# Kernel tuning notes

Hardware: AMD Instinct MI355X
Metric: run time of the kernel (lower is better)

The kernel has to match this reference:

```python
import jax, jax.numpy as jnp
import numpy as np

B, C, H, W = 16, 192, 56, 56
WS = 7; L = WS * WS; NH = 8; HD = C // NH
SHIFTS = (0, 3, 0, 3)  # shift = 0 if i%2==0 else window_size//2


def _ln(x, g, b):
    m = jnp.mean(x, -1, keepdims=True)
    v = jnp.var(x, -1, keepdims=True)
    return (x - m) * jax.lax.rsqrt(v + 1e-5) * g + b


def _win_part(x):
    # (b, H, W, c) -> (b*nW, L, c)
    b, c = x.shape[0], x.shape[-1]
    x = x.reshape(b, H // WS, WS, W // WS, WS, c).transpose(0, 1, 3, 2, 4, 5)
    return x.reshape(-1, L, c)


def _win_rev(xw, b):
    # (b*nW, L, c) -> (b, H, W, c)
    c = xw.shape[-1]
    x = xw.reshape(b, H // WS, W // WS, WS, WS, c).transpose(0, 1, 3, 2, 4, 5)
    return x.reshape(b, H, W, c)


def _rel_index():
    co = np.stack(np.meshgrid(np.arange(WS), np.arange(WS), indexing='ij')).reshape(2, -1)
    r = (co[:, :, None] - co[:, None, :]).transpose(1, 2, 0).astype(np.int64)
    r[..., 0] += WS - 1; r[..., 1] += WS - 1; r[..., 0] *= 2 * WS - 1
    return r.sum(-1)  # (L, L)

REL_IDX = _rel_index()


def _mask(shift):
    if shift == 0:
        return None
    img = np.zeros((1, H, W, 1), np.float32)
    cnt = 0.0
    sl = (slice(0, H - WS), slice(H - WS, H - shift), slice(H - shift, None))
    for hs in sl:
        for ws_ in sl:
            img[:, hs, ws_, :] = cnt
            cnt += 1.0
    mw = np.asarray(_win_part(jnp.asarray(img))).reshape(-1, L)
    am = mw[:, None, :] - mw[:, :, None]
    return jnp.asarray(np.where(am != 0, -100.0, 0.0).astype(np.float32))  # (nW, L, L)

MASKS = [_mask(s) for s in SHIFTS]


def _block(x, n1g, n1b, qw, qb, pw, pb, tab, n2g, n2b, f1w, f1b, f2w, f2b, shift, mask):
    b = x.shape[0]
    sc = x
    x = _ln(x, n1g, n1b)
    if shift:
        x = jnp.roll(x, (-shift, -shift), (1, 2))
    xw = _win_part(x)  # (b*nW, L, C)
    qkv = (xw @ qw.T + qb).reshape(-1, L, 3, NH, HD).transpose(2, 0, 3, 1, 4)
    q, k, v = qkv[0], qkv[1], qkv[2]  # (nB, NH, L, HD)
    attn = jnp.einsum('bhid,bhjd->bhij', q * (HD ** -0.5), k)
    attn = attn + tab[REL_IDX].transpose(2, 0, 1)  # relative position bias (NH, L, L)
    if mask is not None:
        nW = mask.shape[0]
        attn = (attn.reshape(b, nW, NH, L, L) + mask[None, :, None]).reshape(-1, NH, L, L)
    attn = jax.nn.softmax(attn, -1)
    out = jnp.einsum('bhij,bhjd->bhid', attn, v).transpose(0, 2, 1, 3).reshape(-1, L, C)
    out = out @ pw.T + pb
    x = _win_rev(out, b)
    if shift:
        x = jnp.roll(x, (shift, shift), (1, 2))
    x = sc + x
    y = _ln(x, n2g, n2b)
    y = jax.nn.gelu(y @ f1w.T + f1b, approximate=False) @ f2w.T + f2b
    return x + y


def _conv_bn_relu(x, w, b, g, bt, m, v):
    x = jax.lax.conv_general_dilated(x, w, (1, 1), ((1, 1), (1, 1)),
                                     dimension_numbers=('NCHW', 'OIHW', 'NCHW'))
    x = x + b[None, :, None, None]
    x = (x - m[None, :, None, None]) * jax.lax.rsqrt(v + 1e-5)[None, :, None, None]
    x = x * g[None, :, None, None] + bt[None, :, None, None]
    return jax.nn.relu(x)


def setup_inputs() -> dict:
    key = jax.random.key(0)
    ks = iter(jax.random.split(key, 48))
    rn = lambda shape, s=0.02: jax.random.normal(next(ks), shape, jnp.float32) * s
    OD = 96
    return dict(
        x=jax.random.normal(next(ks), (B, C, H, W), jnp.float32),
        pos_embed=rn((1, H * W, C)),
        proj_w=rn((C, C)), proj_b=jnp.zeros((C,)),
        pe_g=jnp.ones((C,)), pe_b=jnp.zeros((C,)),
        n1_g=jnp.ones((4, C)), n1_b=jnp.zeros((4, C)),
        qkv_w=rn((4, 3 * C, C)), qkv_b=jnp.zeros((4, 3 * C)),
        attn_pw=rn((4, C, C)), attn_pb=jnp.zeros((4, C)),
        rel_tab=rn((4, (2 * WS - 1) ** 2, NH)),
        n2_g=jnp.ones((4, C)), n2_b=jnp.zeros((4, C)),
        fc1_w=rn((4, 4 * C, C)), fc1_b=jnp.zeros((4, 4 * C)),
        fc2_w=rn((4, C, 4 * C)), fc2_b=jnp.zeros((4, C)),
        c1_w=rn((C, C, 3, 3)), c1_b=jnp.zeros((C,)),
        bn1_g=jnp.ones((C,)), bn1_b=jnp.zeros((C,)), bn1_m=rn((C,), 0.1), bn1_v=jnp.ones((C,)),
        c2_w=rn((OD, C, 3, 3)), c2_b=jnp.zeros((OD,)),
        bn2_g=jnp.ones((OD,)), bn2_b=jnp.zeros((OD,)), bn2_m=rn((OD,), 0.1), bn2_v=jnp.ones((OD,)),
    )


def reference(x, pos_embed, proj_w, proj_b, pe_g, pe_b, n1_g, n1_b, qkv_w, qkv_b,
              attn_pw, attn_pb, rel_tab, n2_g, n2_b, fc1_w, fc1_b, fc2_w, fc2_b,
              c1_w, c1_b, bn1_g, bn1_b, bn1_m, bn1_v,
              c2_w, c2_b, bn2_g, bn2_b, bn2_m, bn2_v):
    # PatchEmbedding: 1x1 conv == per-pixel linear, then LN, + pos embed
    t = jnp.einsum('bchw,dc->bhwd', x, proj_w) + proj_b  # (B, H, W, D)
    t = _ln(t.reshape(B, H * W, C), pe_g, pe_b) + pos_embed
    o = t.reshape(B, H, W, C)
    for i in range(4):
        o = _block(o, n1_g[i], n1_b[i], qkv_w[i], qkv_b[i], attn_pw[i], attn_pb[i],
                   rel_tab[i], n2_g[i], n2_b[i], fc1_w[i], fc1_b[i], fc2_w[i], fc2_b[i],
                   SHIFTS[i], MASKS[i])
    ds2 = o.transpose(0, 3, 1, 2)  # (B, C, H, W)
    h1 = _conv_bn_relu(ds2, c1_w, c1_b, bn1_g, bn1_b, bn1_m, bn1_v)
    conv_out = _conv_bn_relu(h1, c2_w, c2_b, bn2_g, bn2_b, bn2_m, bn2_v)
    return (conv_out, ds2)
```

## Files before the change

kernel.cpp:

```cpp
#include <hip/hip_runtime.h>
#include <math.h>

typedef unsigned short u16;
typedef unsigned int u32;
typedef __attribute__((ext_vector_type(8))) short short8;
typedef __attribute__((ext_vector_type(4))) float f32x4;

#define IMG 56
#define HW_ 3136
#define NTOK 50176
#define C_DIM 192
#define CONV_OUT_SZ 4816896

__device__ inline float bf2f(u16 v) {
  u32 u = ((u32)v) << 16; float f; __builtin_memcpy(&f, &u, 4); return f;
}
__device__ inline u16 f2bf(float f) {
  u32 u; __builtin_memcpy(&u, &f, 4);
  u += 0x7FFF + ((u >> 16) & 1);
  return (u16)(u >> 16);
}
__device__ inline void glds16(const u16* g, u16* l) {
  __builtin_amdgcn_global_load_lds((const __attribute__((address_space(1))) u32*)g,
                                   (__attribute__((address_space(3))) u32*)l, 16, 0, 0);
}
__device__ inline u32 pk_bf16(float a, float b) {
  u32 r;
  asm("v_cvt_pk_bf16_f32 %0, %1, %2" : "=v"(r) : "v"(a), "v"(b));
  return r;
}

template<int AMODE, int EPI>
__global__ __launch_bounds__(256) void gmm(
    const u16* __restrict__ A, const u16* __restrict__ W,
    const float* __restrict__ bias, void* __restrict__ Cout,
    int M, int N, int K,
    const float* __restrict__ bg, const float* __restrict__ bb,
    const float* __restrict__ bm, const float* __restrict__ bv, int shiftp)
{
  __shared__ u16 As[128 * 64];
  __shared__ u16 Bs[64 * 64];
  const int tid = threadIdx.x;
  const int m0 = blockIdx.x * 128, n0 = blockIdx.y * 64;
  const int lane = tid & 63, wid = tid >> 6;
  const int wm = (wid >> 1) * 64, wn = (wid & 1) * 32;
  const int fr = lane & 15, fg = lane >> 4;
  f32x4 acc[4][2] = {};

  for (int kc = 0; kc < K; kc += 64) {
    #pragma unroll
    for (int it = 0; it < 2; ++it) {
      const int g = it * 256 + tid;
      const int row = g >> 3, cb = (g & 7) << 4;
      const int sc = cb ^ ((row & 7) << 4);
      glds16(W + (size_t)(n0 + row) * K + kc + (sc >> 1), Bs + g * 8);
    }
    if (AMODE == 0) {
      #pragma unroll
      for (int it = 0; it < 4; ++it) {
        const int g = it * 256 + tid;
        const int row = g >> 3, cb = (g & 7) << 4;
        const int sc = cb ^ ((row & 7) << 4);
        glds16(A + (size_t)(m0 + row) * K + kc + (sc >> 1), As + g * 8);
      }
    } else {
      #pragma unroll
      for (int it = 0; it < 4; ++it) {
        const int g = it * 256 + tid;
        const int row = g >> 3, cb = (g & 7) << 4;
        const int m = m0 + row;
        const int b = m / HW_, pp = m - b * HW_;
        const int y = pp / IMG, x = pp - (pp / IMG) * IMG;
        const int kg = kc + (cb >> 1);
        const int s = kg / C_DIM, ic = kg - s * C_DIM;
        const int yy = y + s / 3 - 1, xx = x + (s % 3) - 1;
        short8 v = {0, 0, 0, 0, 0, 0, 0, 0};
        if ((unsigned)yy < IMG && (unsigned)xx < IMG)
          v = *(const short8*)(A + ((size_t)(b * HW_ + yy * IMG + xx)) * C_DIM + ic);
        *(short8*)(As + row * 64 + ((cb ^ ((row & 7) << 4)) >> 1)) = v;
      }
    }
    __syncthreads();
    #pragma unroll
    for (int ks = 0; ks < 2; ++ks) {
      const int kb = ks * 64 + fg * 16;
      short8 af[4], bf[2];
      #pragma unroll
      for (int i = 0; i < 4; ++i) {
        const int row = wm + i * 16 + fr;
        af[i] = *(const short8*)(As + ((row * 128 + (kb ^ ((row & 7) << 4))) >> 1));
      }
      #pragma unroll
      for (int j = 0; j < 2; ++j) {
        const int row = wn + j * 16 + fr;
        bf[j] = *(const short8*)(Bs + ((row * 128 + (kb ^ ((row & 7) << 4))) >> 1));
      }
      #pragma unroll
      for (int i = 0; i < 4; ++i)
        #pragma unroll
        for (int j = 0; j < 2; ++j)
          acc[i][j] = __builtin_amdgcn_mfma_f32_16x16x32_bf16(af[i], bf[j], acc[i][j], 0, 0, 0);
    }
    __syncthreads();
  }

  const int c0 = n0 + wn + fr;
  const int c1i = (EPI == 4) ? min(c0 + 16, N - 1) : (c0 + 16);
  const float bias0 = bias[c0], bias1 = bias[c1i];
  float s0 = 0.f, h0 = 0.f, s1 = 0.f, h1 = 0.f;
  if (EPI == 3 || EPI == 4) {
    s0 = bg[c0] * rsqrtf(bv[c0] + 1e-5f); h0 = bb[c0] - bm[c0] * s0;
    s1 = bg[c1i] * rsqrtf(bv[c1i] + 1e-5f); h1 = bb[c1i] - bm[c1i] * s1;
  }
  #pragma unroll
  for (int i = 0; i < 4; ++i) {
    #pragma unroll
    for (int r = 0; r < 4; ++r) {
      const int m = m0 + wm + i * 16 + fg * 4 + r;
      size_t sbase = 0;
      if (EPI == 6) {
        const int wno = m / 49, within = m - wno * 49;
        const int b2 = wno >> 6, wb3 = wno & 63;
        const int wr = within / 7, wc = within - wr * 7;
        int y2 = (wb3 >> 3) * 7 + wr + shiftp; if (y2 >= IMG) y2 -= IMG;
        int x2 = (wb3 & 7) * 7 + wc + shiftp; if (x2 >= IMG) x2 -= IMG;
        sbase = ((size_t)(b2 * HW_ + y2 * IMG + x2)) * C_DIM;
      }
      #pragma unroll
      for (int j = 0; j < 2; ++j) {
        const int c = c0 + j * 16;
        float v = acc[i][j][r] + (j ? bias1 : bias0);
        if (EPI == 1) v = 0.5f * v * (1.f + erff(v * 0.70710678118f));
        if (EPI == 3 || EPI == 4) { v = v * (j ? s1 : s0) + (j ? h1 : h0); v = fmaxf(v, 0.f); }
        if (EPI == 0 || EPI == 1 || EPI == 3) {
          ((u16*)Cout)[(size_t)m * N + c] = f2bf(v);
        } else if (EPI == 5) {
          ((float*)Cout)[(size_t)m * N + c] = v;
        } else if (EPI == 2) {
          ((float*)Cout)[(size_t)m * N + c] += v;
        } else if (EPI == 6) {
          ((float*)Cout)[sbase + c] += v;
        } else {
          if (c < N) {
            const int b = m / HW_, pp = m - b * HW_;
            ((float*)Cout)[((size_t)b * N + c) * HW_ + pp] = v;
          }
        }
      }
    }
  }
}

__device__ inline void stv(float* p, float v) { *p = v; }
__device__ inline void stv(u16* p, float v) { *p = f2bf(v); }

template<typename OT>
__global__ __launch_bounds__(256) void ln_k(
    const float* __restrict__ in, OT* __restrict__ outp,
    const float* __restrict__ g, const float* __restrict__ bta,
    const float* __restrict__ pos, int winpart, int shift)
{
  const int t = blockIdx.x * 4 + (threadIdx.x >> 6);
  const int lane = threadIdx.x & 63;
  const float* xr = in + (size_t)t * C_DIM;
  const float v0 = xr[lane], v1 = xr[lane + 64], v2 = xr[lane + 128];
  float s = v0 + v1 + v2;
  float ss = v0 * v0 + v1 * v1 + v2 * v2;
  #pragma unroll
  for (int off = 32; off > 0; off >>= 1) {
    s += __shfl_xor(s, off);
    ss += __shfl_xor(ss, off);
  }
  const float mean = s * (1.f / 192.f);
  const float inv = rsqrtf(ss * (1.f / 192.f) - mean * mean + 1e-5f);
  const int b = t / HW_, pp = t - b * HW_;
  size_t obase;
  if (winpart) {
    const int y = pp / IMG, x = pp - (pp / IMG) * IMG;
    int yr = y - shift; if (yr < 0) yr += IMG;
    int xs = x - shift; if (xs < 0) xs += IMG;
    const int win = b * 64 + (yr / 7) * 8 + (xs / 7);
    const int within = (yr % 7) * 7 + (xs % 7);
    obase = ((size_t)win * 49 + within) * C_DIM;
  } else {
    obase = (size_t)t * C_DIM;
  }
  OT* o = outp + obase;
  float p0 = 0.f, p1 = 0.f, p2 = 0.f;
  if (pos) {
    const float* pr = pos + (size_t)pp * C_DIM;
    p0 = pr[lane]; p1 = pr[lane + 64]; p2 = pr[lane + 128];
  }
  stv(o + lane,       (v0 - mean) * inv * g[lane]       + bta[lane]       + p0);
  stv(o + lane + 64,  (v1 - mean) * inv * g[lane + 64]  + bta[lane + 64]  + p1);
  stv(o + lane + 128, (v2 - mean) * inv * g[lane + 128] + bta[lane + 128] + p2);
}

template<int SHIFT>
__global__ __launch_bounds__(256) void attn_m(
    const u16* __restrict__ qkv, u16* __restrict__ outp,
    const float* __restrict__ rel)
{
  __shared__ u16 VT[128 * 64];
  __shared__ float relS[4 * 176 + 16];
  const int tid = threadIdx.x;
  const int wid = tid >> 6, lane = tid & 63;
  const int fr = lane & 15, fg = lane >> 4;
  const int win = blockIdx.x >> 1;
  const int hb = blockIdx.x & 1;
  const int h = hb * 4 + wid;
  const u16* wbase = qkv + (size_t)win * 49 * 576;

  {
    u32* vz = (u32*)VT;
    #pragma unroll
    for (int it = 0; it < 16; ++it) vz[it * 256 + tid] = 0;
  }
  for (int id = tid; id < 169 * 4; id += 256) {
    const int hl = id & 3, ridx = id >> 2;
    relS[hl * 176 + ridx] = rel[ridx * 8 + hb * 4 + hl];
  }
  __syncthreads();
  for (int id = tid; id < 49 * 24; id += 256) {
    const int j = id / 24, dq = id - (id / 24) * 24;
    const int dd = dq * 4;
    const uint2 v = *(const uint2*)(wbase + j * 576 + 384 + hb * 96 + dd);
    const u16* pv = (const u16*)&v;
    const int wpr = dd / 24, dl = dd - wpr * 24;
    #pragma unroll
    for (int e = 0; e < 4; ++e) {
      const int row = wpr * 32 + dl + e;
      VT[(row * 128 + ((j * 2) ^ (((row >> 2) & 7) << 4))) >> 1] = pv[e];
    }
  }
  __syncthreads();

  short8 qf[4], kf[4];
  #pragma unroll
  for (int t = 0; t < 4; ++t) {
    const int row = t * 16 + fr;
    if (fg < 3) {
      qf[t] = *(const short8*)(wbase + row * 576 + h * 24 + fg * 8);
      kf[t] = *(const short8*)(wbase + row * 576 + 192 + h * 24 + fg * 8);
    } else {
      qf[t] = (short8){0, 0, 0, 0, 0, 0, 0, 0};
      kf[t] = (short8){0, 0, 0, 0, 0, 0, 0, 0};
    }
  }

  short8 av[2][2];
  #pragma unroll
  for (int db = 0; db < 2; ++db) {
    const int row = wid * 32 + db * 16 + fr;
    const int swz = ((row >> 2) & 7) << 4;
    #pragma unroll
    for (int ks = 0; ks < 2; ++ks) {
      const uint2 lo = *(const uint2*)((const char*)VT + row * 128 + (((2 * ks) * 32 + fg * 8) ^ swz));
      const uint2 hi = *(const uint2*)((const char*)VT + row * 128 + (((2 * ks + 1) * 32 + fg * 8) ^ swz));
      u32 w[4] = {lo.x, lo.y, hi.x, hi.y};
      av[db][ks] = *(short8*)w;
    }
  }

  const int wb2 = win & 63;
  const int hblk = wb2 >> 3, wblk = wb2 & 7;

  u32 joffPk[4];
  u32 jregPk[2] = {0, 0};
  #pragma unroll
  for (int nj = 0; nj < 4; ++nj) {
    u32 w = 0;
    #pragma unroll
    for (int r = 0; r < 4; ++r) {
      const int j = nj * 16 + fg * 4 + r;
      const int r2 = j / 7, c2 = j - r2 * 7;
      w |= (u32)(r2 * 13 + c2) << (r * 8);
      if (SHIFT) {
        const int hj = hblk * 7 + r2, wj = wblk * 7 + c2;
        const int rj = (hj < 49 ? 0 : (hj < 53 ? 1 : 2)) * 3 + (wj < 49 ? 0 : (wj < 53 ? 1 : 2));
        jregPk[nj >> 1] |= (u32)rj << (((nj & 1) * 4 + r) * 4);
      }
    }
    joffPk[nj] = w;
  }

  const float* relw = relS + wid * 176;
  const float scl = 0.20412414523193154f;

  #pragma unroll
  for (int mi = 0; mi < 4; ++mi) {
    f32x4 sacc[4];
    #pragma unroll
    for (int nj = 0; nj < 4; ++nj)
      sacc[nj] = __builtin_amdgcn_mfma_f32_16x16x32_bf16(kf[nj], qf[mi],
                                                         (f32x4){0, 0, 0, 0}, 0, 0, 0);
    const int i = mi * 16 + fr;
    const int r1 = i / 7, c1 = i - r1 * 7;
    const int base13 = (r1 + 6) * 13 + (c1 + 6);
    int ri = 0;
    if (SHIFT) {
      const int hi2 = hblk * 7 + r1, wi2 = wblk * 7 + c1;
      ri = (hi2 < 49 ? 0 : (hi2 < 53 ? 1 : 2)) * 3 + (wi2 < 49 ? 0 : (wi2 < 53 ? 1 : 2));
    }
    float p[16];
    float mx = -1e30f;
    #pragma unroll
    for (int nj = 0; nj < 4; ++nj) {
      #pragma unroll
      for (int r = 0; r < 4; ++r) {
        const int j = nj * 16 + fg * 4 + r;
        int idx = base13 - (int)((joffPk[nj] >> (r * 8)) & 0xff);
        idx = min(max(idx, 0), 168);
        float v = sacc[nj][r] * scl + relw[idx];
        if (SHIFT) {
          const int rj = (jregPk[nj >> 1] >> (((nj & 1) * 4 + r) * 4)) & 0xf;
          v = (ri != rj) ? v - 100.f : v;
        }
        v = (j < 49) ? v : -1e30f;
        p[nj * 4 + r] = v;
        mx = fmaxf(mx, v);
      }
    }
    mx = fmaxf(mx, __shfl_xor(mx, 16));
    mx = fmaxf(mx, __shfl_xor(mx, 32));
    float sum = 0.f;
    #pragma unroll
    for (int e = 0; e < 16; ++e) { p[e] = __expf(p[e] - mx); sum += p[e]; }
    sum += __shfl_xor(sum, 16);
    sum += __shfl_xor(sum, 32);
    const float inv = 1.f / sum;
    short8 pb[2];
    #pragma unroll
    for (int ks = 0; ks < 2; ++ks) {
      u32 w[4];
      #pragma unroll
      for (int half = 0; half < 2; ++half) {
        const int nj = 2 * ks + half;
        w[half * 2 + 0] = pk_bf16(p[nj * 4 + 0] * inv, p[nj * 4 + 1] * inv);
        w[half * 2 + 1] = pk_bf16(p[nj * 4 + 2] * inv, p[nj * 4 + 3] * inv);
      }
      pb[ks] = *(short8*)w;
    }
    f32x4 o0 = {0, 0, 0, 0}, o1 = {0, 0, 0, 0};
    o0 = __builtin_amdgcn_mfma_f32_16x16x32_bf16(av[0][0], pb[0], o0, 0, 0, 0);
    o0 = __builtin_amdgcn_mfma_f32_16x16x32_bf16(av[0][1], pb[1], o0, 0, 0, 0);
    o1 = __builtin_amdgcn_mfma_f32_16x16x32_bf16(av[1][0], pb[0], o1, 0, 0, 0);
    o1 = __builtin_amdgcn_mfma_f32_16x16x32_bf16(av[1][1], pb[1], o1, 0, 0, 0);
    if (i < 49) {
      u16* orow = outp + ((size_t)win * 49 + i) * C_DIM + h * 24;
      *(uint2*)(orow + fg * 4) =
          make_uint2(pk_bf16(o0[0], o0[1]), pk_bf16(o0[2], o0[3]));
      if (fg < 2)
        *(uint2*)(orow + 16 + fg * 4) =
            make_uint2(pk_bf16(o1[0], o1[1]), pk_bf16(o1[2], o1[3]));
    }
  }
}

__global__ __launch_bounds__(256) void transpose_k(
    const float* __restrict__ in, float* __restrict__ outp)
{
  __shared__ float tile[32][33];
  const int p0 = blockIdx.x * 32;
  const int c0 = blockIdx.y * 32;
  const int tid = threadIdx.x;
  #pragma unroll
  for (int it = 0; it < 4; ++it) {
    const int id = tid + it * 256;
    const int r = id >> 5, cc = id & 31;
    tile[r][cc] = in[(size_t)(p0 + r) * C_DIM + c0 + cc];
  }
  __syncthreads();
  const int b = p0 / HW_, pp0 = p0 - b * HW_;
  #pragma unroll
  for (int it = 0; it < 4; ++it) {
    const int id = tid + it * 256;
    const int cl = id >> 5, pl = id & 31;
    outp[((size_t)b * C_DIM + c0 + cl) * HW_ + pp0 + pl] = tile[pl][cl];
  }
}

__global__ __launch_bounds__(256) void tok_k(
    const float* __restrict__ in, u16* __restrict__ outp)
{
  __shared__ float tile[32][33];
  const int t0 = blockIdx.x * 32;
  const int c0 = blockIdx.y * 32;
  const int tid = threadIdx.x;
  const int b = t0 / HW_, p0 = t0 - b * HW_;
  #pragma unroll
  for (int it = 0; it < 4; ++it) {
    const int id = tid + it * 256;
    const int cl = id >> 5, pl = id & 31;
    tile[cl][pl] = in[((size_t)b * C_DIM + c0 + cl) * HW_ + p0 + pl];
  }
  __syncthreads();
  #pragma unroll
  for (int it = 0; it < 4; ++it) {
    const int id = tid + it * 256;
    const int r = id >> 5, cc = id & 31;
    outp[(size_t)(t0 + r) * C_DIM + c0 + cc] = f2bf(tile[cc][r]);
  }
}

__global__ __launch_bounds__(256) void cvt_k(
    const float* __restrict__ in, u16* __restrict__ outp, int n4)
{
  const int i = blockIdx.x * 256 + threadIdx.x;
  if (i >= n4) return;
  const float4 v = ((const float4*)in)[i];
  u32 lo = (u32)f2bf(v.x) | ((u32)f2bf(v.y) << 16);
  u32 hi = (u32)f2bf(v.z) | ((u32)f2bf(v.w) << 16);
  ((uint2*)outp)[i] = make_uint2(lo, hi);
}

__global__ __launch_bounds__(256) void cvtconv_k(
    const float* __restrict__ src, u16* __restrict__ dst, int OC, int OCpad)
{
  const int idx = blockIdx.x * 256 + threadIdx.x;
  if (idx >= OCpad * 1728) return;
  const int n = idx / 1728, kkk = idx - n * 1728;
  const int s = kkk / C_DIM, ic = kkk - s * C_DIM;
  dst[idx] = (n < OC) ? f2bf(src[((size_t)n * C_DIM + ic) * 9 + s]) : (u16)0;
}

extern "C" void kernel_launch(void* const* d_in, const int* in_sizes, int n_in,
                              void* d_out, int out_size, void* d_ws, size_t ws_size,
                              hipStream_t stream)
{
  const float* x       = (const float*)d_in[0];
  const float* pos     = (const float*)d_in[1];
  const float* proj_w  = (const float*)d_in[2];
  const float* proj_b  = (const float*)d_in[3];
  const float* pe_g    = (const float*)d_in[4];
  const float* pe_b    = (const float*)d_in[5];
  const float* n1_g    = (const float*)d_in[6];
  const float* n1_b    = (const float*)d_in[7];
  const float* qkv_w   = (const float*)d_in[8];
  const float* qkv_b   = (const float*)d_in[9];
  const float* attn_pw = (const float*)d_in[10];
  const float* attn_pb = (const float*)d_in[11];
  const float* rel_tab = (const float*)d_in[12];
  const float* n2_g    = (const float*)d_in[13];
  const float* n2_b    = (const float*)d_in[14];
  const float* fc1_w   = (const float*)d_in[15];
  const float* fc1_b   = (const float*)d_in[16];
  const float* fc2_w   = (const float*)d_in[17];
  const float* fc2_b   = (const float*)d_in[18];
  const float* c1_w    = (const float*)d_in[19];
  const float* c1_b    = (const float*)d_in[20];
  const float* bn1_g   = (const float*)d_in[21];
  const float* bn1_b   = (const float*)d_in[22];
  const float* bn1_m   = (const float*)d_in[23];
  const float* bn1_v   = (const float*)d_in[24];
  const float* c2_w    = (const float*)d_in[25];
  const float* c2_b    = (const float*)d_in[26];
  const float* bn2_g   = (const float*)d_in[27];
  const float* bn2_b   = (const float*)d_in[28];
  const float* bn2_m   = (const float*)d_in[29];
  const float* bn2_v   = (const float*)d_in[30];
  float* out = (float*)d_out;

  const size_t BUF  = (size_t)NTOK * C_DIM * 4;
  const size_t BIGB = (size_t)NTOK * 576 * 2;
  char* ws = (char*)d_ws;
  float* act   = (float*)ws;
  u16*   big16 = (u16*)(ws + BUF);
  float* big32 = (float*)(ws + BUF);
  u16*   xln   = (u16*)(ws + BUF + BIGB);
  u16* attn_out = (u16*)d_out;
  u16* wbf = (u16*)((char*)d_out + (size_t)CONV_OUT_SZ * 4);

  const size_t O_QKV = 0;
  const size_t O_FC1 = O_QKV + (size_t)4 * 576 * 192;
  const size_t O_FC2 = O_FC1 + (size_t)4 * 768 * 192;
  const size_t O_PW  = O_FC2 + (size_t)4 * 192 * 768;
  const size_t O_PROJ= O_PW  + (size_t)4 * 192 * 192;
  const size_t O_C1  = O_PROJ+ (size_t)192 * 192;
  const size_t O_C2  = O_C1  + (size_t)192 * 1728;

  const dim3 blk(256);

  cvt_k<<<(4*576*192/4 + 255)/256, blk, 0, stream>>>(qkv_w,   wbf + O_QKV, 4*576*192/4);
  cvt_k<<<(4*768*192/4 + 255)/256, blk, 0, stream>>>(fc1_w,   wbf + O_FC1, 4*768*192/4);
  cvt_k<<<(4*192*768/4 + 255)/256, blk, 0, stream>>>(fc2_w,   wbf + O_FC2, 4*192*768/4);
  cvt_k<<<(4*192*192/4 + 255)/256, blk, 0, stream>>>(attn_pw, wbf + O_PW,  4*192*192/4);
  cvt_k<<<(192*192/4   + 255)/256, blk, 0, stream>>>(proj_w,  wbf + O_PROJ, 192*192/4);
  cvtconv_k<<<(192*1728 + 255)/256, blk, 0, stream>>>(c1_w, wbf + O_C1, 192, 192);
  cvtconv_k<<<(128*1728 + 255)/256, blk, 0, stream>>>(c2_w, wbf + O_C2, 96, 128);

  tok_k<<<dim3(1568, 6), blk, 0, stream>>>(x, xln);
  gmm<0, 5><<<dim3(392, 3), blk, 0, stream>>>(
      xln, wbf + O_PROJ, proj_b, big32, NTOK, 192, 192,
      nullptr, nullptr, nullptr, nullptr, 0);
  ln_k<float><<<12544, blk, 0, stream>>>(big32, act, pe_g, pe_b, pos, 0, 0);

  for (int i = 0; i < 4; ++i) {
    const int shift = (i & 1) ? 3 : 0;
    ln_k<u16><<<12544, blk, 0, stream>>>(act, xln, n1_g + i * 192, n1_b + i * 192,
                                         nullptr, 1, shift);
    gmm<0, 0><<<dim3(392, 9), blk, 0, stream>>>(
        xln, wbf + O_QKV + (size_t)i * 576 * 192, qkv_b + i * 576, big16,
        NTOK, 576, 192, nullptr, nullptr, nullptr, nullptr, 0);
    if (shift)
      attn_m<3><<<2048, blk, 0, stream>>>(big16, attn_out, rel_tab + i * 169 * 8);
    else
      attn_m<0><<<2048, blk, 0, stream>>>(big16, attn_out, rel_tab + i * 169 * 8);
    gmm<0, 6><<<dim3(392, 3), blk, 0, stream>>>(
        attn_out, wbf + O_PW + (size_t)i * 192 * 192, attn_pb + i * 192, act,
        NTOK, 192, 192, nullptr, nullptr, nullptr, nullptr, shift);
    ln_k<u16><<<12544, blk, 0, stream>>>(act, xln, n2_g + i * 192, n2_b + i * 192,
                                         nullptr, 0, 0);
    for (int c = 0; c < 2; ++c) {
      gmm<0, 1><<<dim3(196, 12), blk, 0, stream>>>(
          xln + (size_t)c * 25088 * 192, wbf + O_FC1 + (size_t)i * 768 * 192,
          fc1_b + i * 768, big16, 25088, 768, 192,
          nullptr, nullptr, nullptr, nullptr, 0);
      gmm<0, 2><<<dim3(196, 3), blk, 0, stream>>>(
          big16, wbf + O_FC2 + (size_t)i * 192 * 768, fc2_b + i * 192,
          act + (size_t)c * 25088 * 192, 25088, 192, 768,
          nullptr, nullptr, nullptr, nullptr, 0);
    }
  }

  cvt_k<<<(NTOK * C_DIM / 4 + 255)/256, blk, 0, stream>>>(act, xln, NTOK * C_DIM / 4);
  gmm<1, 3><<<dim3(392, 3), blk, 0, stream>>>(
      xln, wbf + O_C1, c1_b, big16, NTOK, 192, 1728, bn1_g, bn1_b, bn1_m, bn1_v, 0);
  gmm<1, 4><<<dim3(392, 2), blk, 0, stream>>>(
      big16, wbf + O_C2, c2_b, out, NTOK, 96, 1728, bn2_g, bn2_b, bn2_m, bn2_v, 0);
  transpose_k<<<dim3(1568, 6), blk, 0, stream>>>(act, out + CONV_OUT_SZ);
}
```

Measured before the change: 927.8 us.

## Double-buffer GEMM LDS tiles, stage bf16 epilogue via LDS, merge weight conversions

The GEMM kernel now keeps two LDS buffers for A and B. The next K-tile is issued before computing the current one, and the im2col conv path holds its loads in registers and writes them to LDS after compute. This hides global load latency and halves the barriers. For bf16-output epilogues, results are written to swizzled LDS and then stored as 16-byte vectors instead of scattered 2-byte stores. The seven weight-conversion launches are merged into one kernel. LDS use doubles, which may reduce occupancy.

```diff
diff --git a/kernel.cpp b/kernel.cpp
--- a/kernel.cpp
+++ b/kernel.cpp
@@ -11,6 +11,14 @@
 #define NTOK 50176
 #define C_DIM 192
 #define CONV_OUT_SZ 4816896
+
+#define SZ_QKV (4*576*192)
+#define SZ_FC1 (4*768*192)
+#define SZ_FC2 (4*192*768)
+#define SZ_PW  (4*192*192)
+#define SZ_PROJ (192*192)
+#define SZ_C1R (192*1728)
+#define SZ_C2R (128*1728)
 
 __device__ inline float bf2f(u16 v) {
   u32 u = ((u32)v) << 16; float f; __builtin_memcpy(&f, &u, 4); return f;
@@ -38,71 +46,102 @@
     const float* __restrict__ bg, const float* __restrict__ bb,
     const float* __restrict__ bm, const float* __restrict__ bv, int shiftp)
 {
-  __shared__ u16 As[128 * 64];
-  __shared__ u16 Bs[64 * 64];
+  __shared__ u16 As[2][128 * 64];
+  __shared__ u16 Bs[2][64 * 64];
   const int tid = threadIdx.x;
   const int m0 = blockIdx.x * 128, n0 = blockIdx.y * 64;
   const int lane = tid & 63, wid = tid >> 6;
   const int wm = (wid >> 1) * 64, wn = (wid & 1) * 32;
   const int fr = lane & 15, fg = lane >> 4;
   f32x4 acc[4][2] = {};
-
-  for (int kc = 0; kc < K; kc += 64) {
+  short8 cst0, cst1, cst2, cst3;
+
+  const int nt = K >> 6;
+
+  auto stageB = [&](int kc, int bs) {
     #pragma unroll
     for (int it = 0; it < 2; ++it) {
       const int g = it * 256 + tid;
       const int row = g >> 3, cb = (g & 7) << 4;
       const int sc = cb ^ ((row & 7) << 4);
-      glds16(W + (size_t)(n0 + row) * K + kc + (sc >> 1), Bs + g * 8);
-    }
-    if (AMODE == 0) {
-      #pragma unroll
-      for (int it = 0; it < 4; ++it) {
-        const int g = it * 256 + tid;
-        const int row = g >> 3, cb = (g & 7) << 4;
-        const int sc = cb ^ ((row & 7) << 4);
-        glds16(A + (size_t)(m0 + row) * K + kc + (sc >> 1), As + g * 8);
-      }
-    } else {
-      #pragma unroll
-      for (int it = 0; it < 4; ++it) {
-        const int g = it * 256 + tid;
-        const int row = g >> 3, cb = (g & 7) << 4;
-        const int m = m0 + row;
-        const int b = m / HW_, pp = m - b * HW_;
-        const int y = pp / IMG, x = pp - (pp / IMG) * IMG;
-        const int kg = kc + (cb >> 1);
-        const int s = kg / C_DIM, ic = kg - s * C_DIM;
-        const int yy = y + s / 3 - 1, xx = x + (s % 3) - 1;
-        short8 v = {0, 0, 0, 0, 0, 0, 0, 0};
-        if ((unsigned)yy < IMG && (unsigned)xx < IMG)
-          v = *(const short8*)(A + ((size_t)(b * HW_ + yy * IMG + xx)) * C_DIM + ic);
-        *(short8*)(As + row * 64 + ((cb ^ ((row & 7) << 4)) >> 1)) = v;
-      }
-    }
-    __syncthreads();
+      glds16(W + (size_t)(n0 + row) * K + kc + (sc >> 1), Bs[bs] + g * 8);
+    }
+  };
+  auto stageA = [&](int kc, int bs) {
+    #pragma unroll
+    for (int it = 0; it < 4; ++it) {
+      const int g = it * 256 + tid;
+      const int row = g >> 3, cb = (g & 7) << 4;
+      const int sc = cb ^ ((row & 7) << 4);
+      glds16(A + (size_t)(m0 + row) * K + kc + (sc >> 1), As[bs] + g * 8);
+    }
+  };
+  auto convLoad1 = [&](int kc, int it) {
+    const int g = it * 256 + tid;
+    const int row = g >> 3, cb = (g & 7) << 4;
+    const int m = m0 + row;
+    const int b = m / HW_, pp = m - b * HW_;
+    const int y = pp / IMG, x = pp - (pp / IMG) * IMG;
+    const int kg = kc + (cb >> 1);
+    const int s = kg / C_DIM, ic = kg - s * C_DIM;
+    const int yy = y + s / 3 - 1, xx = x + (s % 3) - 1;
+    short8 v = {0, 0, 0, 0, 0, 0, 0, 0};
+    if ((unsigned)yy < IMG && (unsigned)xx < IMG)
+      v = *(const short8*)(A + ((size_t)(b * HW_ + yy * IMG + xx)) * C_DIM + ic);
+    return v;
+  };
+  auto convLoad = [&](int kc) {
+    cst0 = convLoad1(kc, 0); cst1 = convLoad1(kc, 1);
+    cst2 = convLoad1(kc, 2); cst3 = convLoad1(kc, 3);
+  };
+  auto convWr1 = [&](int bs, int it, short8 v) {
+    const int g = it * 256 + tid;
+    const int row = g >> 3, cb = (g & 7) << 4;
+    *(short8*)(As[bs] + row * 64 + ((cb ^ ((row & 7) << 4)) >> 1)) = v;
+  };
+  auto convWrite = [&](int bs) {
+    convWr1(bs, 0, cst0); convWr1(bs, 1, cst1);
+    convWr1(bs, 2, cst2); convWr1(bs, 3, cst3);
+  };
+  auto compute = [&](int bs) {
     #pragma unroll
     for (int ks = 0; ks < 2; ++ks) {
       const int kb = ks * 64 + fg * 16;
-      short8 af[4], bf[2];
+      short8 af[4], bfv[2];
       #pragma unroll
       for (int i = 0; i < 4; ++i) {
         const int row = wm + i * 16 + fr;
-        af[i] = *(const short8*)(As + ((row * 128 + (kb ^ ((row & 7) << 4))) >> 1));
+        af[i] = *(const short8*)(As[bs] + ((row * 128 + (kb ^ ((row & 7) << 4))) >> 1));
       }
       #pragma unroll
       for (int j = 0; j < 2; ++j) {
         const int row = wn + j * 16 + fr;
-        bf[j] = *(const short8*)(Bs + ((row * 128 + (kb ^ ((row & 7) << 4))) >> 1));
+        bfv[j] = *(const short8*)(Bs[bs] + ((row * 128 + (kb ^ ((row & 7) << 4))) >> 1));
       }
       #pragma unroll
       for (int i = 0; i < 4; ++i)
         #pragma unroll
         for (int j = 0; j < 2; ++j)
-          acc[i][j] = __builtin_amdgcn_mfma_f32_16x16x32_bf16(af[i], bf[j], acc[i][j], 0, 0, 0);
-    }
+          acc[i][j] = __builtin_amdgcn_mfma_f32_16x16x32_bf16(af[i], bfv[j], acc[i][j], 0, 0, 0);
+    }
+  };
+
+  stageB(0, 0);
+  if (AMODE == 0) stageA(0, 0);
+  else { convLoad(0); convWrite(0); }
+  __syncthreads();
+  int buf = 0;
+  for (int t = 0; t < nt - 1; ++t) {
+    const int kc = (t + 1) << 6;
+    stageB(kc, buf ^ 1);
+    if (AMODE == 0) stageA(kc, buf ^ 1);
+    else convLoad(kc);
+    compute(buf);
+    if (AMODE == 1) convWrite(buf ^ 1);
     __syncthreads();
-  }
+    buf ^= 1;
+  }
+  compute(buf);
 
   const int c0 = n0 + wn + fr;
   const int c1i = (EPI == 4) ? min(c0 + 16, N - 1) : (c0 + 16);
@@ -112,38 +151,65 @@
     s0 = bg[c0] * rsqrtf(bv[c0] + 1e-5f); h0 = bb[c0] - bm[c0] * s0;
     s1 = bg[c1i] * rsqrtf(bv[c1i] + 1e-5f); h1 = bb[c1i] - bm[c1i] * s1;
   }
-  #pragma unroll
-  for (int i = 0; i < 4; ++i) {
-    #pragma unroll
-    for (int r = 0; r < 4; ++r) {
-      const int m = m0 + wm + i * 16 + fg * 4 + r;
-      size_t sbase = 0;
-      if (EPI == 6) {
-        const int wno = m / 49, within = m - wno * 49;
-        const int b2 = wno >> 6, wb3 = wno & 63;
-        const int wr = within / 7, wc = within - wr * 7;
-        int y2 = (wb3 >> 3) * 7 + wr + shiftp; if (y2 >= IMG) y2 -= IMG;
-        int x2 = (wb3 & 7) * 7 + wc + shiftp; if (x2 >= IMG) x2 -= IMG;
-        sbase = ((size_t)(b2 * HW_ + y2 * IMG + x2)) * C_DIM;
+
+  if (EPI == 0 || EPI == 1 || EPI == 3) {
+    __syncthreads();
+    u16* T = &As[0][0];
+    #pragma unroll
+    for (int i = 0; i < 4; ++i) {
+      #pragma unroll
+      for (int r = 0; r < 4; ++r) {
+        const int ml = wm + i * 16 + fg * 4 + r;
+        #pragma unroll
+        for (int j = 0; j < 2; ++j) {
+          float v = acc[i][j][r] + (j ? bias1 : bias0);
+          if (EPI == 1) v = 0.5f * v * (1.f + erff(v * 0.70710678118f));
+          if (EPI == 3) { v = v * (j ? s1 : s0) + (j ? h1 : h0); v = fmaxf(v, 0.f); }
+          const int cl = wn + j * 16 + fr;
+          T[ml * 64 + ((cl & 7) | ((((cl >> 3) ^ ml) & 7) << 3))] = f2bf(v);
+        }
       }
+    }
+    __syncthreads();
+    #pragma unroll
+    for (int p = 0; p < 4; ++p) {
+      const int id = p * 256 + tid;
+      const int ml = id >> 3, g = id & 7;
+      const int pg = (g ^ ml) & 7;
+      *(short8*)((u16*)Cout + (size_t)(m0 + ml) * N + n0 + g * 8) =
+          *(const short8*)(T + ml * 64 + pg * 8);
+    }
+  } else {
+    #pragma unroll
+    for (int i = 0; i < 4; ++i) {
       #pragma unroll
-      for (int j = 0; j < 2; ++j) {
-        const int c = c0 + j * 16;
-        float v = acc[i][j][r] + (j ? bias1 : bias0);
-        if (EPI == 1) v = 0.5f * v * (1.f + erff(v * 0.70710678118f));
-        if (EPI == 3 || EPI == 4) { v = v * (j ? s1 : s0) + (j ? h1 : h0); v = fmaxf(v, 0.f); }
-        if (EPI == 0 || EPI == 1 || EPI == 3) {
-          ((u16*)Cout)[(size_t)m * N + c] = f2bf(v);
-        } else if (EPI == 5) {
-          ((float*)Cout)[(size_t)m * N + c] = v;
-        } else if (EPI == 2) {
-          ((float*)Cout)[(size_t)m * N + c] += v;
-        } else if (EPI == 6) {
-          ((float*)Cout)[sbase + c] += v;
-        } else {
-          if (c < N) {
-            const int b = m / HW_, pp = m - b * HW_;
-            ((float*)Cout)[((size_t)b * N + c) * HW_ + pp] = v;
+      for (int r = 0; r < 4; ++r) {
+        const int m = m0 + wm + i * 16 + fg * 4 + r;
+        size_t sbase = 0;
+        if (EPI == 6) {
+          const int wno = m / 49, within = m - wno * 49;
+          const int b2 = wno >> 6, wb3 = wno & 63;
+          const int wr = within / 7, wc = within - wr * 7;
+          int y2 = (wb3 >> 3) * 7 + wr + shiftp; if (y2 >= IMG) y2 -= IMG;
+          int x2 = (wb3 & 7) * 7 + wc + shiftp; if (x2 >= IMG) x2 -= IMG;
+          sbase = ((size_t)(b2 * HW_ + y2 * IMG + x2)) * C_DIM;
+        }
+        #pragma unroll
+        for (int j = 0; j < 2; ++j) {
+          const int c = c0 + j * 16;
+          float v = acc[i][j][r] + (j ? bias1 : bias0);
+          if (EPI == 4) { v = v * (j ? s1 : s0) + (j ? h1 : h0); v = fmaxf(v, 0.f); }
+          if (EPI == 5) {
+            ((float*)Cout)[(size_t)m * N + c] = v;
+          } else if (EPI == 2) {
+            ((float*)Cout)[(size_t)m * N + c] += v;
+          } else if (EPI == 6) {
+            ((float*)Cout)[sbase + c] += v;
+          } else {
+            if (c < N) {
+              const int b = m / HW_, pp = m - b * HW_;
+              ((float*)Cout)[((size_t)b * N + c) * HW_ + pp] = v;
+            }
           }
         }
       }
@@ -414,14 +480,35 @@
   ((uint2*)outp)[i] = make_uint2(lo, hi);
 }
 
-__global__ __launch_bounds__(256) void cvtconv_k(
-    const float* __restrict__ src, u16* __restrict__ dst, int OC, int OCpad)
-{
-  const int idx = blockIdx.x * 256 + threadIdx.x;
-  if (idx >= OCpad * 1728) return;
-  const int n = idx / 1728, kkk = idx - n * 1728;
-  const int s = kkk / C_DIM, ic = kkk - s * C_DIM;
-  dst[idx] = (n < OC) ? f2bf(src[((size_t)n * C_DIM + ic) * 9 + s]) : (u16)0;
+__global__ __launch_bounds__(256) void cvtall_k(
+    const float* __restrict__ qkv_w, const float* __restrict__ fc1_w,
+    const float* __restrict__ fc2_w, const float* __restrict__ attn_pw,
+    const float* __restrict__ proj_w, const float* __restrict__ c1_w,
+    const float* __restrict__ c2_w, u16* __restrict__ wbf)
+{
+  const int i = blockIdx.x * 256 + threadIdx.x;
+  const int off1 = SZ_QKV, off2 = off1 + SZ_FC1, off3 = off2 + SZ_FC2,
+            off4 = off3 + SZ_PW, off5 = off4 + SZ_PROJ, off6 = off5 + SZ_C1R,
+            off7 = off6 + SZ_C2R;
+  if (i >= off7) return;
+  float v;
+  if (i < off1) v = qkv_w[i];
+  else if (i < off2) v = fc1_w[i - off1];
+  else if (i < off3) v = fc2_w[i - off2];
+  else if (i < off4) v = attn_pw[i - off3];
+  else if (i < off5) v = proj_w[i - off4];
+  else if (i < off6) {
+    const int e = i - off5;
+    const int n = e / 1728, kkk = e - n * 1728;
+    const int s = kkk / C_DIM, ic = kkk - s * C_DIM;
+    v = c1_w[((size_t)n * C_DIM + ic) * 9 + s];
+  } else {
+    const int e = i - off6;
+    const int n = e / 1728, kkk = e - n * 1728;
+    const int s = kkk / C_DIM, ic = kkk - s * C_DIM;
+    v = (n < 96) ? c2_w[((size_t)n * C_DIM + ic) * 9 + s] : 0.f;
+  }
+  wbf[i] = f2bf(v);
 }
 
 extern "C" void kernel_launch(void* const* d_in, const int* in_sizes, int n_in,
@@ -472,22 +559,18 @@
   u16* wbf = (u16*)((char*)d_out + (size_t)CONV_OUT_SZ * 4);
 
   const size_t O_QKV = 0;
-  const size_t O_FC1 = O_QKV + (size_t)4 * 576 * 192;
-  const size_t O_FC2 = O_FC1 + (size_t)4 * 768 * 192;
-  const size_t O_PW  = O_FC2 + (size_t)4 * 192 * 768;
-  const size_t O_PROJ= O_PW  + (size_t)4 * 192 * 192;
-  const size_t O_C1  = O_PROJ+ (size_t)192 * 192;
-  const size_t O_C2  = O_C1  + (size_t)192 * 1728;
+  const size_t O_FC1 = O_QKV + SZ_QKV;
+  const size_t O_FC2 = O_FC1 + SZ_FC1;
+  const size_t O_PW  = O_FC2 + SZ_FC2;
+  const size_t O_PROJ= O_PW  + SZ_PW;
+  const size_t O_C1  = O_PROJ+ SZ_PROJ;
+  const size_t O_C2  = O_C1  + SZ_C1R;
 
   const dim3 blk(256);
 
-  cvt_k<<<(4*576*192/4 + 255)/256, blk, 0, stream>>>(qkv_w,   wbf + O_QKV, 4*576*192/4);
-  cvt_k<<<(4*768*192/4 + 255)/256, blk, 0, stream>>>(fc1_w,   wbf + O_FC1, 4*768*192/4);
-  cvt_k<<<(4*192*768/4 + 255)/256, blk, 0, stream>>>(fc2_w,   wbf + O_FC2, 4*192*768/4);
-  cvt_k<<<(4*192*192/4 + 255)/256, blk, 0, stream>>>(attn_pw, wbf + O_PW,  4*192*192/4);
-  cvt_k<<<(192*192/4   + 255)/256, blk, 0, stream>>>(proj_w,  wbf + O_PROJ, 192*192/4);
-  cvtconv_k<<<(192*1728 + 255)/256, blk, 0, stream>>>(c1_w, wbf + O_C1, 192, 192);
-  cvtconv_k<<<(128*1728 + 255)/256, blk, 0, stream>>>(c2_w, wbf + O_C2, 96, 128);
+  const int cvtall_n = SZ_QKV + SZ_FC1 + SZ_FC2 + SZ_PW + SZ_PROJ + SZ_C1R + SZ_C2R;
+  cvtall_k<<<(cvtall_n + 255) / 256, blk, 0, stream>>>(
+      qkv_w, fc1_w, fc2_w, attn_pw, proj_w, c1_w, c2_w, wbf);
 
   tok_k<<<dim3(1568, 6), blk, 0, stream>>>(x, xln);
   gmm<0, 5><<<dim3(392, 3), blk, 0, stream>>>(
```

New measurement: 1.009 ms. +8.7%, slower.
